# Kernel tuning notes

Measured on AMD Instinct MI355X. Metric: run time of the kernel, lower is better.

## Reference

```python
import jax, jax.numpy as jnp
import numpy as np

N, S, D = 16, 32, 256      # batch, seq_len, hidden_size
B = 4                      # sample_size (Monte-Carlo beams)
CH = 4 * D                 # cell_hidden_dim = 4*hidden (hard-coded in __init__)
EPS = 1e-20


def _ln(x, g, b):
    m = x.mean(-1, keepdims=True)
    v = ((x - m) ** 2).mean(-1, keepdims=True)
    return (x - m) / jnp.sqrt(v + 1e-5) * g + b


def _masked_softmax(logits, mask):
    p = jax.nn.softmax(logits, axis=-1)
    p = p * mask + EPS
    return p / p.sum(-1, keepdims=True)


def _cell(l, r, w1, b1, w2, b2, ln2_g, ln2_b):
    # TreeLSTM-style fused cell: Linear -> GELU -> Linear -> gates -> LayerNorm
    cat = jnp.concatenate([l, r], axis=-1)                  # (NB, s, 2D)
    inter = jax.nn.gelu(cat @ w1 + b1, approximate=False)   # (NB, s, 4D)
    contents = (inter @ w2 + b2).reshape(*l.shape[:-1], 4, D)
    gates = jax.nn.sigmoid(contents[..., 0:3, :])
    f1, f2, ig = gates[..., 0, :], gates[..., 1, :], gates[..., 2, :]
    parent = contents[..., 3, :]
    return _ln(f1 * l + f2 * r + ig * parent, ln2_g, ln2_b)


def _select(old_h, new_h, mask, accu, dec_W, dec_b, key):
    NB, Sc, Dd = new_h.shape
    old_l, old_r = old_h[:, :-1], old_h[:, 1:]
    nh = new_h * mask[:, :, None]
    pad = jnp.zeros((NB, 1, Dd), nh.dtype)
    l1 = jnp.concatenate([pad, nh[:, :-1]], axis=1)
    l2 = jnp.concatenate([pad, l1[:, :-1]], axis=1)
    r1 = jnp.concatenate([nh[:, 1:], pad], axis=1)
    r2 = jnp.concatenate([r1[:, 1:], pad], axis=1)
    win = jnp.concatenate([l2, l1, nh, r1, r2], axis=-1)    # (NB, Sc, 5D)
    logits = (win @ dec_W + dec_b)[..., 0] / np.sqrt(5 * Dd)
    # straight-through Gumbel softmax (temperature = 1)
    u = jax.random.uniform(key, logits.shape, logits.dtype)
    g = -jnp.log(-jnp.log(u + EPS) + EPS)
    y_soft = _masked_softmax(logits + g, mask)
    y_hard = jax.nn.one_hot(jnp.argmax(y_soft, axis=-1), Sc, dtype=y_soft.dtype)
    sel = jax.lax.stop_gradient(y_hard - y_soft) + y_soft
    soft_scores = jnp.sum(sel * _masked_softmax(logits, mask), axis=1)
    accu = accu + jnp.log(soft_scores + EPS)
    cs = jnp.cumsum(sel, axis=1)
    left = (1.0 - cs)[:, :, None]
    right = (cs - sel)[:, :, None]
    merged = sel[:, :, None] * new_h + left * old_l + right * old_r
    return merged, accu


def setup_inputs() -> dict:
    key = jax.random.key(0)
    ks = jax.random.split(key, 6)
    f32 = jnp.float32
    return {
        "x": jax.random.normal(ks[0], (N, S, D), f32),
        "input_mask": jnp.ones((N, S), f32),
        "word_W": jax.random.normal(ks[1], (D, D), f32) / np.sqrt(D),
        "word_b": jnp.zeros((D,), f32),
        "ln_g": jnp.ones((D,), f32),
        "ln_b": jnp.zeros((D,), f32),
        "w1": jax.random.normal(ks[2], (2 * D, CH), f32) / np.sqrt(2 * D),
        "b1": jnp.zeros((CH,), f32),
        "w2": jax.random.normal(ks[3], (CH, 4 * D), f32) / np.sqrt(CH),
        "b2": jnp.zeros((4 * D,), f32),
        "ln2_g": jnp.ones((D,), f32),
        "ln2_b": jnp.zeros((D,), f32),
        "dec_W": jax.random.normal(ks[4], (5 * D, 1), f32) / np.sqrt(5 * D),
        "dec_b": jnp.zeros((1,), f32),
    }


def reference(x, input_mask, word_W, word_b, ln_g, ln_b, w1, b1, w2, b2,
              ln2_g, ln2_b, dec_W, dec_b):
    state = _ln(x @ word_W + word_b, ln_g, ln_b)                 # (N, S, D)
    state = jnp.repeat(state[:, None], B, axis=1).reshape(N * B, S, D)
    lmask = jnp.repeat(input_mask[:, None], B, axis=1).reshape(N * B, S)
    accu = jnp.zeros((N * B,), state.dtype)
    base = jax.random.key(1234)
    # sequential tree-building recurrence; sequence axis shrinks by 1 each step
    for i in range(S - 1):
        l, r = state[:, :-1], state[:, 1:]
        new_state = _cell(l, r, w1, b1, w2, b2, ln2_g, ln2_b)
        if i < S - 2:
            new_state, new_accu = _select(state, new_state, lmask[:, i + 1:],
                                          accu, dec_W, dec_b,
                                          jax.random.fold_in(base, i))
        else:
            new_accu = accu
        done = lmask[:, i + 1]
        state = done[:, None, None] * new_state + (1.0 - done[:, None, None]) * state[:, :-1]
        accu = done * new_accu + (1.0 - done) * accu
    h = state[:, 0].reshape(N, B, D)
    scores = jax.nn.softmax(accu.reshape(N, B, 1), axis=1)
    return jnp.sum(scores * h, axis=1)                            # (N, D)
```

## Files before the change

### kernel.cpp

```cpp
#include <hip/hip_runtime.h>
#include <cstdint>
#include <cstddef>

namespace {
constexpr int kP0 = 31;
constexpr int kM0 = 496;
}

__device__ float g_state[2][64 * 32 * 256];
__device__ float g_nh[2][64 * kP0 * 256];
__device__ float g_s5[2][64 * kP0 * 5];
__device__ float g_nh0[kM0 * 256];
__device__ float g_s50[kM0 * 5];
__device__ float g_inter0[(size_t)kM0 * 1024];
__device__ float g_cont0[(size_t)kM0 * 1024];
__device__ float g_p1[4][128 * 1024];
__device__ float g_p2[4][128 * 1024];
__device__ float g_accu[64];
__device__ int g_slots[2][128];

__device__ __forceinline__ void tf2x32(uint32_t k0, uint32_t k1, uint32_t x0,
                                       uint32_t x1, uint32_t& o0, uint32_t& o1) {
  uint32_t ks2 = k0 ^ k1 ^ 0x1BD11BDAu;
  x0 += k0; x1 += k1;
#define TF_ROT(v, r) (((v) << (r)) | ((v) >> (32 - (r))))
#define TF_RD(r) { x0 += x1; x1 = TF_ROT(x1, r); x1 ^= x0; }
  TF_RD(13) TF_RD(15) TF_RD(26) TF_RD(6)   x0 += k1;  x1 += ks2 + 1u;
  TF_RD(17) TF_RD(29) TF_RD(16) TF_RD(24)  x0 += ks2; x1 += k0 + 2u;
  TF_RD(13) TF_RD(15) TF_RD(26) TF_RD(6)   x0 += k0;  x1 += k1 + 3u;
  TF_RD(17) TF_RD(29) TF_RD(16) TF_RD(24)  x0 += k1;  x1 += ks2 + 4u;
  TF_RD(13) TF_RD(15) TF_RD(26) TF_RD(6)   x0 += ks2; x1 += k0 + 5u;
  o0 = x0; o1 = x1;
#undef TF_RD
#undef TF_ROT
}

__device__ __forceinline__ float blockSum256(float v, float* red4, int tid) {
#pragma unroll
  for (int o = 32; o > 0; o >>= 1) v += __shfl_down(v, o, 64);
  __syncthreads();
  if ((tid & 63) == 0) red4[tid >> 6] = v;
  __syncthreads();
  return red4[0] + red4[1] + red4[2] + red4[3];
}
__device__ __forceinline__ float waveMax64(float v) {
#pragma unroll
  for (int o = 32; o > 0; o >>= 1) v = fmaxf(v, __shfl_xor(v, o, 64));
  return v;
}
__device__ __forceinline__ float waveSum64(float v) {
#pragma unroll
  for (int o = 32; o > 0; o >>= 1) v += __shfl_xor(v, o, 64);
  return v;
}
__device__ __forceinline__ float geluf(float v) {
  return 0.5f * v * (1.0f + erff(v * 0.70710678118654752440f));
}

__global__ __launch_bounds__(256) void k_embed(const float* __restrict__ x,
                                               const float* __restrict__ wW,
                                               const float* __restrict__ wb,
                                               const float* __restrict__ lng,
                                               const float* __restrict__ lnb) {
  int row = blockIdx.x;
  int d = threadIdx.x;
  __shared__ float xs[256];
  __shared__ float red4[4];
  xs[d] = x[row * 256 + d];
  __syncthreads();
  float acc = wb[d];
  for (int k = 0; k < 256; ++k) acc = fmaf(xs[k], wW[k * 256 + d], acc);
  float mean = blockSum256(acc, red4, d) * (1.0f / 256.0f);
  float cen = acc - mean;
  float var = blockSum256(cen * cen, red4, d) * (1.0f / 256.0f);
  float o = cen / sqrtf(var + 1e-5f) * lng[d] + lnb[d];
  int n = row >> 5, s = row & 31;
#pragma unroll
  for (int bb = 0; bb < 4; ++bb)
    g_state[0][((n * 4 + bb) * 32 + s) * 256 + d] = o;
  if (row == 0 && d < 64) g_accu[d] = 0.0f;
}


__global__ __launch_bounds__(128) void k_g1s(const float* __restrict__ w1,
                                             const float* __restrict__ b1) {
  __shared__ float As[64][20];
  __shared__ float Ws[64][132];
  const int tid = threadIdx.x;
  const int colB = blockIdx.x * 128;
  const int rowB = blockIdx.y * 16;
  const int rg = tid >> 5, cgp = tid & 31;
  const int ar = tid & 15, kq = tid >> 4;
  const int wc = tid & 31, wk = tid >> 5;
  const float* Ab;
  {
    int m = rowB + ar;
    int n = m / 31, j = m - n * 31;
    Ab = g_state[0] + (n * 4) * 8192 + j * 256;
  }
  float acc[4][4] = {};
  for (int c = 0; c < 8; ++c) {
    const int kb = c * 64;
#pragma unroll
    for (int q = 0; q < 2; ++q) {
      int kp = kq * 8 + q * 4;
      float4 a = *(const float4*)&Ab[kb + kp];
      As[kp + 0][ar] = a.x; As[kp + 1][ar] = a.y;
      As[kp + 2][ar] = a.z; As[kp + 3][ar] = a.w;
    }
#pragma unroll
    for (int q = 0; q < 16; ++q) {
      int kk = wk * 16 + q;
      *(float4*)&Ws[kk][wc * 4] =
          *(const float4*)&w1[(size_t)(kb + kk) * 1024 + colB + wc * 4];
    }
    __syncthreads();
#pragma unroll
    for (int kk = 0; kk < 64; ++kk) {
      float4 a4 = *(const float4*)&As[kk][rg * 4];
      float4 w4 = *(const float4*)&Ws[kk][cgp * 4];
      float av[4] = {a4.x, a4.y, a4.z, a4.w};
      float wv[4] = {w4.x, w4.y, w4.z, w4.w};
#pragma unroll
      for (int ri = 0; ri < 4; ++ri)
#pragma unroll
        for (int ci = 0; ci < 4; ++ci)
          acc[ri][ci] = fmaf(av[ri], wv[ci], acc[ri][ci]);
    }
    __syncthreads();
  }
  const int col = colB + cgp * 4;
  float4 bb = *(const float4*)&b1[col];
#pragma unroll
  for (int ri = 0; ri < 4; ++ri) {
    int m = rowB + rg * 4 + ri;
    float4 o;
    o.x = geluf(acc[ri][0] + bb.x); o.y = geluf(acc[ri][1] + bb.y);
    o.z = geluf(acc[ri][2] + bb.z); o.w = geluf(acc[ri][3] + bb.w);
    *(float4*)&g_inter0[(size_t)m * 1024 + col] = o;
  }
}

__global__ __launch_bounds__(128) void k_g2s(const float* __restrict__ w2) {
  __shared__ float As[64][20];
  __shared__ float Ws[64][132];
  const int tid = threadIdx.x;
  const int colB = blockIdx.x * 128;
  const int rowB = blockIdx.y * 16;
  const int rg = tid >> 5, cgp = tid & 31;
  const int ar = tid & 15, kq = tid >> 4;
  const int wc = tid & 31, wk = tid >> 5;
  const float* Ab = g_inter0 + (size_t)(rowB + ar) * 1024;
  float acc[4][4] = {};
  for (int c = 0; c < 16; ++c) {
    const int kb = c * 64;
#pragma unroll
    for (int q = 0; q < 2; ++q) {
      int kp = kq * 8 + q * 4;
      float4 a = *(const float4*)&Ab[kb + kp];
      As[kp + 0][ar] = a.x; As[kp + 1][ar] = a.y;
      As[kp + 2][ar] = a.z; As[kp + 3][ar] = a.w;
    }
#pragma unroll
    for (int q = 0; q < 16; ++q) {
      int kk = wk * 16 + q;
      *(float4*)&Ws[kk][wc * 4] =
          *(const float4*)&w2[(size_t)(kb + kk) * 1024 + colB + wc * 4];
    }
    __syncthreads();
#pragma unroll
    for (int kk = 0; kk < 64; ++kk) {
      float4 a4 = *(const float4*)&As[kk][rg * 4];
      float4 w4 = *(const float4*)&Ws[kk][cgp * 4];
      float av[4] = {a4.x, a4.y, a4.z, a4.w};
      float wv[4] = {w4.x, w4.y, w4.z, w4.w};
#pragma unroll
      for (int ri = 0; ri < 4; ++ri)
#pragma unroll
        for (int ci = 0; ci < 4; ++ci)
          acc[ri][ci] = fmaf(av[ri], wv[ci], acc[ri][ci]);
    }
    __syncthreads();
  }
  const int col = colB + cgp * 4;
#pragma unroll
  for (int ri = 0; ri < 4; ++ri) {
    int m = rowB + rg * 4 + ri;
    float4 o = {acc[ri][0], acc[ri][1], acc[ri][2], acc[ri][3]};
    *(float4*)&g_cont0[(size_t)m * 1024 + col] = o;
  }
}

__device__ __forceinline__ float4 g2t_loadA(int grow, int kpos, const float* __restrict__ b1) {
  size_t g = (size_t)grow * 1024 + kpos;
  float4 p0 = *(const float4*)&g_p1[0][g];
  float4 p1 = *(const float4*)&g_p1[1][g];
  float4 p2 = *(const float4*)&g_p1[2][g];
  float4 p3 = *(const float4*)&g_p1[3][g];
  float4 bb = *(const float4*)&b1[kpos];
  float4 r;
  r.x = geluf(p0.x + p1.x + p2.x + p3.x + bb.x);
  r.y = geluf(p0.y + p1.y + p2.y + p3.y + bb.y);
  r.z = geluf(p0.z + p1.z + p2.z + p3.z + bb.z);
  r.w = geluf(p0.w + p1.w + p2.w + p3.w + bb.w);
  return r;
}

__global__ __launch_bounds__(128) void k_g2t(const float* __restrict__ w2,
                                             const float* __restrict__ b1) {
  __shared__ float As[64][36];
  __shared__ float Ws[64][68];
  const int tid = threadIdx.x;
  const int colB = blockIdx.x * 64;
  const int rowB = blockIdx.y * 32;
  const int Ks = blockIdx.z;
  const int kb0 = Ks * 256;
  const int rg = tid >> 4, cgp = tid & 15;
  const int ar = tid & 31, kq = tid >> 5;
  const int wc = tid & 15, wk = tid >> 4;
  const int grow = rowB + ar;
  float acc[4][4] = {};
  for (int c = 0; c < 4; ++c) {
    const int kb = kb0 + c * 64;
#pragma unroll
    for (int q = 0; q < 4; ++q) {
      int kp = kq * 16 + q * 4;
      float4 a = g2t_loadA(grow, kb + kp, b1);
      As[kp + 0][ar] = a.x; As[kp + 1][ar] = a.y;
      As[kp + 2][ar] = a.z; As[kp + 3][ar] = a.w;
    }
#pragma unroll
    for (int q = 0; q < 8; ++q) {
      int kk = wk * 8 + q;
      *(float4*)&Ws[kk][wc * 4] =
          *(const float4*)&w2[(size_t)(kb + kk) * 1024 + colB + wc * 4];
    }
    __syncthreads();
#pragma unroll
    for (int kk = 0; kk < 64; ++kk) {
      float4 a4 = *(const float4*)&As[kk][rg * 4];
      float4 w4 = *(const float4*)&Ws[kk][cgp * 4];
      float av[4] = {a4.x, a4.y, a4.z, a4.w};
      float wv[4] = {w4.x, w4.y, w4.z, w4.w};
#pragma unroll
      for (int ri = 0; ri < 4; ++ri)
#pragma unroll
        for (int ci = 0; ci < 4; ++ci)
          acc[ri][ci] = fmaf(av[ri], wv[ci], acc[ri][ci]);
    }
    __syncthreads();
  }
  const int col = colB + cgp * 4;
#pragma unroll
  for (int ri = 0; ri < 4; ++ri) {
    int r = rowB + rg * 4 + ri;
    float4 o = {acc[ri][0], acc[ri][1], acc[ri][2], acc[ri][3]};
    *(float4*)&g_p2[Ks][r * 1024 + col] = o;
  }
}

__global__ __launch_bounds__(256) void k_cellfull(const float* __restrict__ imask,
                                                  const float* __restrict__ ln2g,
                                                  const float* __restrict__ ln2b,
                                                  const float* __restrict__ decW,
                                                  const float* __restrict__ b2) {
  int m = blockIdx.x;
  int d = threadIdx.x;
  int n = m / 31, j = m - n * 31;
  const float* st = g_state[0] + (n * 4) * 8192;
  const float* crow = g_cont0 + (size_t)m * 1024;
  float c0 = crow[d] + b2[d];
  float c1 = crow[256 + d] + b2[256 + d];
  float c2 = crow[512 + d] + b2[512 + d];
  float c3 = crow[768 + d] + b2[768 + d];
  float l = st[j * 256 + d];
  float r = st[(j + 1) * 256 + d];
  float f1 = 1.0f / (1.0f + expf(-c0));
  float f2 = 1.0f / (1.0f + expf(-c1));
  float ig = 1.0f / (1.0f + expf(-c2));
  float pre = f1 * l + f2 * r + ig * c3;
  __shared__ float red4[4];
  __shared__ float w5[4][5];
  float mean = blockSum256(pre, red4, d) * (1.0f / 256.0f);
  float cen = pre - mean;
  float var = blockSum256(cen * cen, red4, d) * (1.0f / 256.0f);
  float nh = cen / sqrtf(var + 1e-5f) * ln2g[d] + ln2b[d];
  g_nh0[m * 256 + d] = nh;
  float mv = imask[n * 32 + 1 + j];
  float nhm = nh * mv;
  float pv[5];
#pragma unroll
  for (int t = 0; t < 5; ++t) pv[t] = nhm * decW[t * 256 + d];
#pragma unroll
  for (int t = 0; t < 5; ++t)
#pragma unroll
    for (int o = 32; o > 0; o >>= 1) pv[t] += __shfl_down(pv[t], o, 64);
  __syncthreads();
  if ((d & 63) == 0) {
#pragma unroll
    for (int t = 0; t < 5; ++t) w5[d >> 6][t] = pv[t];
  }
  __syncthreads();
  if (d < 5) g_s50[m * 5 + d] = w5[0][d] + w5[1][d] + w5[2][d] + w5[3][d];
}

__global__ __launch_bounds__(256) void k_cm(
    const float* __restrict__ imask, const float* __restrict__ decW,
    const float* __restrict__ decb, const float* __restrict__ b2,
    const float* __restrict__ ln2g, const float* __restrict__ ln2b,
    const float* __restrict__ w1, int i, int last) {
  const int b = blockIdx.x, grp = blockIdx.y;
  const int tid = threadIdx.x, st = tid, lane = tid & 63, wv = tid >> 6;
  const int Sc = 31 - i;
  const int buf = i & 1;
  const int n32 = (b >> 2) * 32;
  __shared__ float sh_nhf[2][256];
  __shared__ float sh_s5f[2][5];
  __shared__ float sA[3][256];
  __shared__ float red4[4];
  __shared__ float w5s[4][5];
  __shared__ int sh_k;
  __shared__ float sh_sv;
  int slot0 = -1, slot1 = -1;
  if (i > 0) { slot0 = g_slots[buf][2 * b]; slot1 = g_slots[buf][2 * b + 1]; }
  const float* s5Src = (i == 0) ? (g_s50 + (b >> 2) * kP0 * 5) : (g_s5[buf] + b * kP0 * 5);
  const float* nhSrcG = (i == 0) ? (g_nh0 + (size_t)(b >> 2) * kP0 * 256)
                                 : (g_nh[buf] + (size_t)b * kP0 * 256);
  const float* stOld = g_state[buf] + b * 8192;
  float* stNew = g_state[(i + 1) & 1] + b * 8192;
  float* nhDst = g_nh[(i + 1) & 1] + (size_t)b * kP0 * 256;
  float* s5Dst = g_s5[(i + 1) & 1] + b * kP0 * 5;
  float done = imask[n32 + i + 1];

  if (i > 0) {
#pragma unroll 1
    for (int s = 0; s < 2; ++s) {
      int j = (s == 0) ? slot0 : slot1;
      if (j < 0) continue;
      int sr = 2 * b + s;
      float c[4];
#pragma unroll
      for (int q = 0; q < 4; ++q) {
        int g = sr * 1024 + q * 256 + st;
        float v = ((g_p2[0][g] + g_p2[1][g]) + g_p2[2][g]) + g_p2[3][g];
        c[q] = v + b2[q * 256 + st];
      }
      float l = stOld[j * 256 + st];
      float r = stOld[(j + 1) * 256 + st];
      float f1 = 1.0f / (1.0f + expf(-c[0]));
      float f2 = 1.0f / (1.0f + expf(-c[1]));
      float ig = 1.0f / (1.0f + expf(-c[2]));
      float pre = f1 * l + f2 * r + ig * c[3];
      float mean = blockSum256(pre, red4, st) * (1.0f / 256.0f);
      float cen = pre - mean;
      float var = blockSum256(cen * cen, red4, st) * (1.0f / 256.0f);
      float nh = cen / sqrtf(var + 1e-5f) * ln2g[st] + ln2b[st];
      sh_nhf[s][st] = nh;
      float mv = imask[n32 + i + 1 + j];
      float nhm = nh * mv;
      float pv[5];
#pragma unroll
      for (int t = 0; t < 5; ++t) pv[t] = nhm * decW[t * 256 + st];
#pragma unroll
      for (int t = 0; t < 5; ++t) {
        float v = pv[t];
#pragma unroll
        for (int o = 32; o > 0; o >>= 1) v += __shfl_down(v, o, 64);
        pv[t] = v;
      }
      __syncthreads();
      if (lane == 0) {
#pragma unroll
        for (int t = 0; t < 5; ++t) w5s[wv][t] = pv[t];
      }
      __syncthreads();
      if (st < 5) sh_s5f[s][st] = w5s[0][st] + w5s[1][st] + w5s[2][st] + w5s[3][st];
    }
  }
  __syncthreads();

  if (!last && tid < 64) {
    int j = lane;
    bool act = j < Sc;
    float mv = 0.f, lg = 0.f;
    if (act) {
      mv = imask[n32 + i + 1 + j];
      float t5 = decb[0];
      if (j >= 2) {
        int rw = j - 2;
        t5 += (i > 0 && rw == slot0) ? sh_s5f[0][0] : (i > 0 && rw == slot1) ? sh_s5f[1][0] : s5Src[rw * 5 + 0];
      }
      if (j >= 1) {
        int rw = j - 1;
        t5 += (i > 0 && rw == slot0) ? sh_s5f[0][1] : (i > 0 && rw == slot1) ? sh_s5f[1][1] : s5Src[rw * 5 + 1];
      }
      {
        int rw = j;
        t5 += (i > 0 && rw == slot0) ? sh_s5f[0][2] : (i > 0 && rw == slot1) ? sh_s5f[1][2] : s5Src[rw * 5 + 2];
      }
      if (j + 1 < Sc) {
        int rw = j + 1;
        t5 += (i > 0 && rw == slot0) ? sh_s5f[0][3] : (i > 0 && rw == slot1) ? sh_s5f[1][3] : s5Src[rw * 5 + 3];
      }
      if (j + 2 < Sc) {
        int rw = j + 2;
        t5 += (i > 0 && rw == slot0) ? sh_s5f[0][4] : (i > 0 && rw == slot1) ? sh_s5f[1][4] : s5Src[rw * 5 + 4];
      }
      lg = t5 / 35.77708763999664f;
    }
    uint32_t fk0, fk1, o0, o1;
    tf2x32(0u, 1234u, 0u, (uint32_t)i, fk0, fk1);
    uint32_t idx = (uint32_t)(b * Sc + j);
    tf2x32(fk0, fk1, 0u, idx, o0, o1);
    uint32_t bits = o0 ^ o1;
    float u = __uint_as_float((bits >> 9) | 0x3f800000u) - 1.0f;
    float gum = -logf(-logf(u + 1e-20f) + 1e-20f);
    float z = lg + gum;
    float zm = waveMax64(act ? z : -3.0e38f);
    float e = act ? expf(z - zm) : 0.f;
    float p = e / waveSum64(e);
    float y = act ? (p * mv + 1e-20f) : 0.f;
    float ys = y / waveSum64(y);
    float av = act ? ys : -1.f;
    int ai = j;
#pragma unroll
    for (int o = 32; o > 0; o >>= 1) {
      float ov = __shfl_xor(av, o, 64);
      int oi = __shfl_xor(ai, o, 64);
      if (ov > av || (ov == av && oi < ai)) { av = ov; ai = oi; }
    }
    float lm = waveMax64(act ? lg : -3.0e38f);
    float e2 = act ? expf(lg - lm) : 0.f;
    float p2 = e2 / waveSum64(e2);
    float y2 = act ? (p2 * mv + 1e-20f) : 0.f;
    float ps = y2 / waveSum64(y2);
    float ysk = __shfl(ys, ai, 64);
    float psk = __shfl(ps, ai, 64);
    float sv = (1.0f - ysk) + ysk;
    if (j == 0) {
      sh_k = ai;
      sh_sv = sv;
      if (grp == 0) {
        g_accu[b] += done * logf(sv * psk + 1e-20f);
        int s0 = -1, s1 = -1;
        if (done != 0.0f) {
          if (ai >= 1) s0 = ai - 1;
          if (ai <= Sc - 2) s1 = ai;
        }
        g_slots[(i + 1) & 1][2 * b] = s0;
        g_slots[(i + 1) & 1][2 * b + 1] = s1;
      }
    }
  }
  __syncthreads();

  if (last) {
    if (grp == 0 && wv == 0) {
      float4 ol = *(const float4*)&stOld[lane * 4];
      float4 nh4;
      if (slot0 == 0) nh4 = *(const float4*)&sh_nhf[0][lane * 4];
      else if (slot1 == 0) nh4 = *(const float4*)&sh_nhf[1][lane * 4];
      else nh4 = *(const float4*)&nhSrcG[lane * 4];
      float4 o4;
      o4.x = done * nh4.x + (1.0f - done) * ol.x;
      o4.y = done * nh4.y + (1.0f - done) * ol.y;
      o4.z = done * nh4.z + (1.0f - done) * ol.z;
      o4.w = done * nh4.w + (1.0f - done) * ol.w;
      *(float4*)&stNew[lane * 4] = o4;
    }
    return;
  }

  int k = sh_k;
  float sv = sh_sv;
#pragma unroll 1
  for (int rr = 0; rr < 2; ++rr) {
    int jrow = grp * 8 + wv * 2 + rr;
    if (jrow >= Sc) continue;
    float4 ol = *(const float4*)&stOld[jrow * 256 + lane * 4];
    float4 ov4;
    if (done != 0.0f) {
      float4 mg;
      if (jrow < k) {
        mg = ol;
      } else if (jrow == k) {
        float4 nh4 = (i > 0 && k == slot0) ? *(const float4*)&sh_nhf[0][lane * 4]
                   : (i > 0 && k == slot1) ? *(const float4*)&sh_nhf[1][lane * 4]
                   : *(const float4*)&nhSrcG[k * 256 + lane * 4];
        mg.x = sv * nh4.x + (1.0f - sv) * ol.x;
        mg.y = sv * nh4.y + (1.0f - sv) * ol.y;
        mg.z = sv * nh4.z + (1.0f - sv) * ol.z;
        mg.w = sv * nh4.w + (1.0f - sv) * ol.w;
      } else {
        float4 orr = *(const float4*)&stOld[(jrow + 1) * 256 + lane * 4];
        mg.x = (1.0f - sv) * ol.x + sv * orr.x;
        mg.y = (1.0f - sv) * ol.y + sv * orr.y;
        mg.z = (1.0f - sv) * ol.z + sv * orr.z;
        mg.w = (1.0f - sv) * ol.w + sv * orr.w;
      }
      ov4.x = done * mg.x + (1.0f - done) * ol.x;
      ov4.y = done * mg.y + (1.0f - done) * ol.y;
      ov4.z = done * mg.z + (1.0f - done) * ol.z;
      ov4.w = done * mg.w + (1.0f - done) * ol.w;
    } else {
      ov4 = ol;
    }
    *(float4*)&stNew[jrow * 256 + lane * 4] = ov4;
    if (jrow < Sc - 1) {
      int src = (done != 0.0f && jrow > k) ? jrow + 1 : jrow;
      float4 nv = (i > 0 && src == slot0) ? *(const float4*)&sh_nhf[0][lane * 4]
                : (i > 0 && src == slot1) ? *(const float4*)&sh_nhf[1][lane * 4]
                : *(const float4*)&nhSrcG[src * 256 + lane * 4];
      *(float4*)&nhDst[jrow * 256 + lane * 4] = nv;
      float mv2 = imask[n32 + i + 2 + jrow];
      float pv[5];
#pragma unroll
      for (int t = 0; t < 5; ++t) {
        const float* dw = decW + t * 256 + lane * 4;
        pv[t] = (nv.x * dw[0] + nv.y * dw[1] + nv.z * dw[2] + nv.w * dw[3]) * mv2;
      }
#pragma unroll
      for (int t = 0; t < 5; ++t) {
        float v = pv[t];
#pragma unroll
        for (int o = 32; o > 0; o >>= 1) v += __shfl_down(v, o, 64);
        pv[t] = v;
      }
      if (lane == 0) {
#pragma unroll
        for (int t = 0; t < 5; ++t) s5Dst[jrow * 5 + t] = pv[t];
      }
    }
  }

  if (done != 0.0f) {
    __syncthreads();
    {
      int d = st;
      float nhKv = (i > 0 && k == slot0) ? sh_nhf[0][d]
                 : (i > 0 && k == slot1) ? sh_nhf[1][d]
                 : nhSrcG[k * 256 + d];
#pragma unroll
      for (int t = 0; t < 3; ++t) {
        int r = k - 1 + t;
        if (r < 0 || r > Sc - 1) continue;
        float ol = stOld[r * 256 + d];
        float mg;
        if (r < k) mg = ol;
        else if (r == k) mg = sv * nhKv + (1.0f - sv) * ol;
        else mg = (1.0f - sv) * ol + sv * stOld[(r + 1) * 256 + d];
        sA[t][d] = done * mg + (1.0f - done) * ol;
      }
    }
    __syncthreads();
    const int Ks = grp;
    const int has0 = (k >= 1);
    const int has1 = (k <= Sc - 2);
    const int kb0 = Ks * 128;
    const float* A0 = (Ks < 2) ? sA[0] : sA[1];
    const float* A1 = (Ks < 2) ? sA[1] : sA[2];
    const int koff = (Ks < 2) ? kb0 : (kb0 - 256);
    const int col = st * 4;
    float a00 = 0.f, a01 = 0.f, a02 = 0.f, a03 = 0.f;
    float a10 = 0.f, a11 = 0.f, a12 = 0.f, a13 = 0.f;
    for (int kk = 0; kk < 128; ++kk) {
      float4 w = *(const float4*)&w1[(size_t)(kb0 + kk) * 1024 + col];
      float av0 = A0[koff + kk];
      float av1 = A1[koff + kk];
      a00 = fmaf(av0, w.x, a00); a01 = fmaf(av0, w.y, a01);
      a02 = fmaf(av0, w.z, a02); a03 = fmaf(av0, w.w, a03);
      a10 = fmaf(av1, w.x, a10); a11 = fmaf(av1, w.y, a11);
      a12 = fmaf(av1, w.z, a12); a13 = fmaf(av1, w.w, a13);
    }
    if (has0) {
      float4 o = {a00, a01, a02, a03};
      *(float4*)&g_p1[Ks][(2 * b + 0) * 1024 + col] = o;
    }
    if (has1) {
      float4 o = {a10, a11, a12, a13};
      *(float4*)&g_p1[Ks][(2 * b + 1) * 1024 + col] = o;
    }
  }
}

__global__ __launch_bounds__(256) void k_final(float* __restrict__ out) {
  int n = blockIdx.x, d = threadIdx.x;
  float a0 = g_accu[n * 4 + 0], a1 = g_accu[n * 4 + 1];
  float a2 = g_accu[n * 4 + 2], a3 = g_accu[n * 4 + 3];
  float mx = fmaxf(fmaxf(a0, a1), fmaxf(a2, a3));
  float e0 = expf(a0 - mx), e1 = expf(a1 - mx), e2 = expf(a2 - mx), e3 = expf(a3 - mx);
  float ssum = e0 + e1 + e2 + e3;
  const float* st1 = g_state[1];
  float h0 = st1[(n * 4 + 0) * 8192 + d];
  float h1 = st1[(n * 4 + 1) * 8192 + d];
  float h2 = st1[(n * 4 + 2) * 8192 + d];
  float h3 = st1[(n * 4 + 3) * 8192 + d];
  out[n * 256 + d] = (e0 / ssum) * h0 + (e1 / ssum) * h1 + (e2 / ssum) * h2 + (e3 / ssum) * h3;
}

extern "C" void kernel_launch(void* const* d_in, const int* in_sizes, int n_in,
                              void* d_out, int out_size, void* d_ws, size_t ws_size,
                              hipStream_t stream) {
  (void)in_sizes; (void)n_in; (void)d_ws; (void)ws_size; (void)out_size;
  const float* x = (const float*)d_in[0];
  const float* imask = (const float*)d_in[1];
  const float* wW = (const float*)d_in[2];
  const float* wb = (const float*)d_in[3];
  const float* lng = (const float*)d_in[4];
  const float* lnb = (const float*)d_in[5];
  const float* w1 = (const float*)d_in[6];
  const float* b1 = (const float*)d_in[7];
  const float* w2 = (const float*)d_in[8];
  const float* b2 = (const float*)d_in[9];
  const float* ln2g = (const float*)d_in[10];
  const float* ln2b = (const float*)d_in[11];
  const float* decW = (const float*)d_in[12];
  const float* decb = (const float*)d_in[13];
  float* out = (float*)d_out;

  k_embed<<<dim3(512), dim3(256), 0, stream>>>(x, wW, wb, lng, lnb);
  k_g1s<<<dim3(8, 31), dim3(128), 0, stream>>>(w1, b1);
  k_g2s<<<dim3(8, 31), dim3(128), 0, stream>>>(w2);
  k_cellfull<<<dim3(kM0), dim3(256), 0, stream>>>(imask, ln2g, ln2b, decW, b2);
  k_cm<<<dim3(64, 4), dim3(256), 0, stream>>>(imask, decW, decb, b2, ln2g, ln2b, w1, 0, 0);
  for (int i = 1; i <= 30; ++i) {
    k_g2t<<<dim3(16, 4, 4), dim3(128), 0, stream>>>(w2, b1);
    int lastf = (i == 30) ? 1 : 0;
    k_cm<<<dim3(64, lastf ? 1 : 4), dim3(256), 0, stream>>>(imask, decW, decb, b2,
                                                            ln2g, ln2b, w1, i, lastf);
  }
  k_final<<<dim3(16), dim3(256), 0, stream>>>(out);
}
```

Before: 1.324 ms.

## Fuse the 30-step tail recurrence into one persistent per-beam kernel

Replaces the 60 per-step launches of k_g2t and k_cm with one k_tail kernel: 64 blocks of 1024 threads, each owning a beam and looping over all 30 steps. Both cell matmuls for the two affected rows run inside the block, with partial sums, the selection scores and the slots kept in shared memory. The step-0 merge goes into a separate k_cm0 kernel. This removes launch overhead and global round-trips between steps, but each step now uses only 64 CUs, and each block re-streams the full w1 and w2 weights every step with little reuse.

Measured after the change: 2.011 ms. 1.52x slower.

```diff
diff --git a/kernel.cpp b/kernel.cpp
--- a/kernel.cpp
+++ b/kernel.cpp
@@ -14,8 +14,6 @@
 __device__ float g_s50[kM0 * 5];
 __device__ float g_inter0[(size_t)kM0 * 1024];
 __device__ float g_cont0[(size_t)kM0 * 1024];
-__device__ float g_p1[4][128 * 1024];
-__device__ float g_p2[4][128 * 1024];
 __device__ float g_accu[64];
 __device__ int g_slots[2][128];
 
@@ -42,6 +40,14 @@
   if ((tid & 63) == 0) red4[tid >> 6] = v;
   __syncthreads();
   return red4[0] + red4[1] + red4[2] + red4[3];
+}
+__device__ __forceinline__ float bs16(float v, float* red16, int tid) {
+#pragma unroll
+  for (int o = 32; o > 0; o >>= 1) v += __shfl_down(v, o, 64);
+  __syncthreads();
+  if ((tid & 63) == 0) red16[tid >> 6] = v;
+  __syncthreads();
+  return red16[0] + red16[1] + red16[2] + red16[3];
 }
 __device__ __forceinline__ float waveMax64(float v) {
 #pragma unroll
@@ -188,74 +194,6 @@
     int m = rowB + rg * 4 + ri;
     float4 o = {acc[ri][0], acc[ri][1], acc[ri][2], acc[ri][3]};
     *(float4*)&g_cont0[(size_t)m * 1024 + col] = o;
-  }
-}
-
-__device__ __forceinline__ float4 g2t_loadA(int grow, int kpos, const float* __restrict__ b1) {
-  size_t g = (size_t)grow * 1024 + kpos;
-  float4 p0 = *(const float4*)&g_p1[0][g];
-  float4 p1 = *(const float4*)&g_p1[1][g];
-  float4 p2 = *(const float4*)&g_p1[2][g];
-  float4 p3 = *(const float4*)&g_p1[3][g];
-  float4 bb = *(const float4*)&b1[kpos];
-  float4 r;
-  r.x = geluf(p0.x + p1.x + p2.x + p3.x + bb.x);
-  r.y = geluf(p0.y + p1.y + p2.y + p3.y + bb.y);
-  r.z = geluf(p0.z + p1.z + p2.z + p3.z + bb.z);
-  r.w = geluf(p0.w + p1.w + p2.w + p3.w + bb.w);
-  return r;
-}
-
-__global__ __launch_bounds__(128) void k_g2t(const float* __restrict__ w2,
-                                             const float* __restrict__ b1) {
-  __shared__ float As[64][36];
-  __shared__ float Ws[64][68];
-  const int tid = threadIdx.x;
-  const int colB = blockIdx.x * 64;
-  const int rowB = blockIdx.y * 32;
-  const int Ks = blockIdx.z;
-  const int kb0 = Ks * 256;
-  const int rg = tid >> 4, cgp = tid & 15;
-  const int ar = tid & 31, kq = tid >> 5;
-  const int wc = tid & 15, wk = tid >> 4;
-  const int grow = rowB + ar;
-  float acc[4][4] = {};
-  for (int c = 0; c < 4; ++c) {
-    const int kb = kb0 + c * 64;
-#pragma unroll
-    for (int q = 0; q < 4; ++q) {
-      int kp = kq * 16 + q * 4;
-      float4 a = g2t_loadA(grow, kb + kp, b1);
-      As[kp + 0][ar] = a.x; As[kp + 1][ar] = a.y;
-      As[kp + 2][ar] = a.z; As[kp + 3][ar] = a.w;
-    }
-#pragma unroll
-    for (int q = 0; q < 8; ++q) {
-      int kk = wk * 8 + q;
-      *(float4*)&Ws[kk][wc * 4] =
-          *(const float4*)&w2[(size_t)(kb + kk) * 1024 + colB + wc * 4];
-    }
-    __syncthreads();
-#pragma unroll
-    for (int kk = 0; kk < 64; ++kk) {
-      float4 a4 = *(const float4*)&As[kk][rg * 4];
-      float4 w4 = *(const float4*)&Ws[kk][cgp * 4];
-      float av[4] = {a4.x, a4.y, a4.z, a4.w};
-      float wv[4] = {w4.x, w4.y, w4.z, w4.w};
-#pragma unroll
-      for (int ri = 0; ri < 4; ++ri)
-#pragma unroll
-        for (int ci = 0; ci < 4; ++ci)
-          acc[ri][ci] = fmaf(av[ri], wv[ci], acc[ri][ci]);
-    }
-    __syncthreads();
-  }
-  const int col = colB + cgp * 4;
-#pragma unroll
-  for (int ri = 0; ri < 4; ++ri) {
-    int r = rowB + rg * 4 + ri;
-    float4 o = {acc[ri][0], acc[ri][1], acc[ri][2], acc[ri][3]};
-    *(float4*)&g_p2[Ks][r * 1024 + col] = o;
   }
 }
 
@@ -304,112 +242,40 @@
   if (d < 5) g_s50[m * 5 + d] = w5[0][d] + w5[1][d] + w5[2][d] + w5[3][d];
 }
 
-__global__ __launch_bounds__(256) void k_cm(
+__global__ __launch_bounds__(256) void k_cm0(
     const float* __restrict__ imask, const float* __restrict__ decW,
-    const float* __restrict__ decb, const float* __restrict__ b2,
-    const float* __restrict__ ln2g, const float* __restrict__ ln2b,
-    const float* __restrict__ w1, int i, int last) {
+    const float* __restrict__ decb, const float* __restrict__ ln2g,
+    const float* __restrict__ ln2b) {
   const int b = blockIdx.x, grp = blockIdx.y;
-  const int tid = threadIdx.x, st = tid, lane = tid & 63, wv = tid >> 6;
-  const int Sc = 31 - i;
-  const int buf = i & 1;
+  const int tid = threadIdx.x, lane = tid & 63, wv = tid >> 6;
+  const int Sc = 31;
   const int n32 = (b >> 2) * 32;
-  __shared__ float sh_nhf[2][256];
-  __shared__ float sh_s5f[2][5];
-  __shared__ float sA[3][256];
-  __shared__ float red4[4];
-  __shared__ float w5s[4][5];
   __shared__ int sh_k;
   __shared__ float sh_sv;
-  int slot0 = -1, slot1 = -1;
-  if (i > 0) { slot0 = g_slots[buf][2 * b]; slot1 = g_slots[buf][2 * b + 1]; }
-  const float* s5Src = (i == 0) ? (g_s50 + (b >> 2) * kP0 * 5) : (g_s5[buf] + b * kP0 * 5);
-  const float* nhSrcG = (i == 0) ? (g_nh0 + (size_t)(b >> 2) * kP0 * 256)
-                                 : (g_nh[buf] + (size_t)b * kP0 * 256);
-  const float* stOld = g_state[buf] + b * 8192;
-  float* stNew = g_state[(i + 1) & 1] + b * 8192;
-  float* nhDst = g_nh[(i + 1) & 1] + (size_t)b * kP0 * 256;
-  float* s5Dst = g_s5[(i + 1) & 1] + b * kP0 * 5;
-  float done = imask[n32 + i + 1];
-
-  if (i > 0) {
-#pragma unroll 1
-    for (int s = 0; s < 2; ++s) {
-      int j = (s == 0) ? slot0 : slot1;
-      if (j < 0) continue;
-      int sr = 2 * b + s;
-      float c[4];
-#pragma unroll
-      for (int q = 0; q < 4; ++q) {
-        int g = sr * 1024 + q * 256 + st;
-        float v = ((g_p2[0][g] + g_p2[1][g]) + g_p2[2][g]) + g_p2[3][g];
-        c[q] = v + b2[q * 256 + st];
-      }
-      float l = stOld[j * 256 + st];
-      float r = stOld[(j + 1) * 256 + st];
-      float f1 = 1.0f / (1.0f + expf(-c[0]));
-      float f2 = 1.0f / (1.0f + expf(-c[1]));
-      float ig = 1.0f / (1.0f + expf(-c[2]));
-      float pre = f1 * l + f2 * r + ig * c[3];
-      float mean = blockSum256(pre, red4, st) * (1.0f / 256.0f);
-      float cen = pre - mean;
-      float var = blockSum256(cen * cen, red4, st) * (1.0f / 256.0f);
-      float nh = cen / sqrtf(var + 1e-5f) * ln2g[st] + ln2b[st];
-      sh_nhf[s][st] = nh;
-      float mv = imask[n32 + i + 1 + j];
-      float nhm = nh * mv;
-      float pv[5];
-#pragma unroll
-      for (int t = 0; t < 5; ++t) pv[t] = nhm * decW[t * 256 + st];
-#pragma unroll
-      for (int t = 0; t < 5; ++t) {
-        float v = pv[t];
-#pragma unroll
-        for (int o = 32; o > 0; o >>= 1) v += __shfl_down(v, o, 64);
-        pv[t] = v;
-      }
-      __syncthreads();
-      if (lane == 0) {
-#pragma unroll
-        for (int t = 0; t < 5; ++t) w5s[wv][t] = pv[t];
-      }
-      __syncthreads();
-      if (st < 5) sh_s5f[s][st] = w5s[0][st] + w5s[1][st] + w5s[2][st] + w5s[3][st];
-    }
-  }
-  __syncthreads();
-
-  if (!last && tid < 64) {
+  const float* s5Src = g_s50 + (b >> 2) * kP0 * 5;
+  const float* nhSrcG = g_nh0 + (size_t)(b >> 2) * kP0 * 256;
+  const float* stOld = g_state[0] + b * 8192;
+  float* stNew = g_state[1] + b * 8192;
+  float* nhDst = g_nh[1] + (size_t)b * kP0 * 256;
+  float* s5Dst = g_s5[1] + b * kP0 * 5;
+  float done = imask[n32 + 1];
+
+  if (tid < 64) {
     int j = lane;
     bool act = j < Sc;
     float mv = 0.f, lg = 0.f;
     if (act) {
-      mv = imask[n32 + i + 1 + j];
+      mv = imask[n32 + 1 + j];
       float t5 = decb[0];
-      if (j >= 2) {
-        int rw = j - 2;
-        t5 += (i > 0 && rw == slot0) ? sh_s5f[0][0] : (i > 0 && rw == slot1) ? sh_s5f[1][0] : s5Src[rw * 5 + 0];
-      }
-      if (j >= 1) {
-        int rw = j - 1;
-        t5 += (i > 0 && rw == slot0) ? sh_s5f[0][1] : (i > 0 && rw == slot1) ? sh_s5f[1][1] : s5Src[rw * 5 + 1];
-      }
-      {
-        int rw = j;
-        t5 += (i > 0 && rw == slot0) ? sh_s5f[0][2] : (i > 0 && rw == slot1) ? sh_s5f[1][2] : s5Src[rw * 5 + 2];
-      }
-      if (j + 1 < Sc) {
-        int rw = j + 1;
-        t5 += (i > 0 && rw == slot0) ? sh_s5f[0][3] : (i > 0 && rw == slot1) ? sh_s5f[1][3] : s5Src[rw * 5 + 3];
-      }
-      if (j + 2 < Sc) {
-        int rw = j + 2;
-        t5 += (i > 0 && rw == slot0) ? sh_s5f[0][4] : (i > 0 && rw == slot1) ? sh_s5f[1][4] : s5Src[rw * 5 + 4];
-      }
+      if (j >= 2) t5 += s5Src[(j - 2) * 5 + 0];
+      if (j >= 1) t5 += s5Src[(j - 1) * 5 + 1];
+      t5 += s5Src[j * 5 + 2];
+      if (j + 1 < Sc) t5 += s5Src[(j + 1) * 5 + 3];
+      if (j + 2 < Sc) t5 += s5Src[(j + 2) * 5 + 4];
       lg = t5 / 35.77708763999664f;
     }
     uint32_t fk0, fk1, o0, o1;
-    tf2x32(0u, 1234u, 0u, (uint32_t)i, fk0, fk1);
+    tf2x32(0u, 1234u, 0u, 0u, fk0, fk1);
     uint32_t idx = (uint32_t)(b * Sc + j);
     tf2x32(fk0, fk1, 0u, idx, o0, o1);
     uint32_t bits = o0 ^ o1;
@@ -447,140 +313,384 @@
           if (ai >= 1) s0 = ai - 1;
           if (ai <= Sc - 2) s1 = ai;
         }
-        g_slots[(i + 1) & 1][2 * b] = s0;
-        g_slots[(i + 1) & 1][2 * b + 1] = s1;
-      }
-    }
-  }
-  __syncthreads();
-
-  if (last) {
-    if (grp == 0 && wv == 0) {
-      float4 ol = *(const float4*)&stOld[lane * 4];
-      float4 nh4;
-      if (slot0 == 0) nh4 = *(const float4*)&sh_nhf[0][lane * 4];
-      else if (slot1 == 0) nh4 = *(const float4*)&sh_nhf[1][lane * 4];
-      else nh4 = *(const float4*)&nhSrcG[lane * 4];
-      float4 o4;
-      o4.x = done * nh4.x + (1.0f - done) * ol.x;
-      o4.y = done * nh4.y + (1.0f - done) * ol.y;
-      o4.z = done * nh4.z + (1.0f - done) * ol.z;
-      o4.w = done * nh4.w + (1.0f - done) * ol.w;
-      *(float4*)&stNew[lane * 4] = o4;
-    }
-    return;
-  }
+        g_slots[1][2 * b] = s0;
+        g_slots[1][2 * b + 1] = s1;
+      }
+    }
+  }
+  __syncthreads();
 
   int k = sh_k;
   float sv = sh_sv;
+  {
+    int jrow = grp * 4 + wv;
+    if (jrow < Sc) {
+      float4 ol = *(const float4*)&stOld[jrow * 256 + lane * 4];
+      float4 ov4;
+      if (done != 0.0f) {
+        float4 mg;
+        if (jrow < k) {
+          mg = ol;
+        } else if (jrow == k) {
+          float4 nh4 = *(const float4*)&nhSrcG[k * 256 + lane * 4];
+          mg.x = sv * nh4.x + (1.0f - sv) * ol.x;
+          mg.y = sv * nh4.y + (1.0f - sv) * ol.y;
+          mg.z = sv * nh4.z + (1.0f - sv) * ol.z;
+          mg.w = sv * nh4.w + (1.0f - sv) * ol.w;
+        } else {
+          float4 orr = *(const float4*)&stOld[(jrow + 1) * 256 + lane * 4];
+          mg.x = (1.0f - sv) * ol.x + sv * orr.x;
+          mg.y = (1.0f - sv) * ol.y + sv * orr.y;
+          mg.z = (1.0f - sv) * ol.z + sv * orr.z;
+          mg.w = (1.0f - sv) * ol.w + sv * orr.w;
+        }
+        ov4.x = done * mg.x + (1.0f - done) * ol.x;
+        ov4.y = done * mg.y + (1.0f - done) * ol.y;
+        ov4.z = done * mg.z + (1.0f - done) * ol.z;
+        ov4.w = done * mg.w + (1.0f - done) * ol.w;
+      } else {
+        ov4 = ol;
+      }
+      *(float4*)&stNew[jrow * 256 + lane * 4] = ov4;
+      if (jrow < Sc - 1) {
+        int src = (done != 0.0f && jrow > k) ? jrow + 1 : jrow;
+        float4 nv = *(const float4*)&nhSrcG[src * 256 + lane * 4];
+        *(float4*)&nhDst[jrow * 256 + lane * 4] = nv;
+        float mv2 = imask[n32 + 2 + jrow];
+        float pv[5];
+#pragma unroll
+        for (int t = 0; t < 5; ++t) {
+          const float* dw = decW + t * 256 + lane * 4;
+          pv[t] = (nv.x * dw[0] + nv.y * dw[1] + nv.z * dw[2] + nv.w * dw[3]) * mv2;
+        }
+#pragma unroll
+        for (int t = 0; t < 5; ++t) {
+          float v = pv[t];
+#pragma unroll
+          for (int o = 32; o > 0; o >>= 1) v += __shfl_down(v, o, 64);
+          pv[t] = v;
+        }
+        if (lane == 0) {
+#pragma unroll
+          for (int t = 0; t < 5; ++t) s5Dst[jrow * 5 + t] = pv[t];
+        }
+      }
+    }
+  }
+}
+
+__global__ __launch_bounds__(1024, 1) void k_tail(
+    const float* __restrict__ imask, const float* __restrict__ decW,
+    const float* __restrict__ decb, const float* __restrict__ b1,
+    const float* __restrict__ b2, const float* __restrict__ ln2g,
+    const float* __restrict__ ln2b, const float* __restrict__ w1,
+    const float* __restrict__ w2) {
+  const int b = blockIdx.x;
+  const int tid = threadIdx.x;
+  const int lane = tid & 63, wv = tid >> 6;
+  const int n32 = (b >> 2) * 32;
+  __shared__ float S[4][2][1024];
+  __shared__ float IC[2][1024];
+  __shared__ float As2[2][512];
+  __shared__ float sh_nhf[2][256];
+  __shared__ float sh_s5f[2][5];
+  __shared__ float s5buf[2][32][5];
+  __shared__ float red16[16];
+  __shared__ float w5s[4][5];
+  __shared__ int sh_slot0, sh_slot1;
+  __shared__ int sh_k;
+  __shared__ float sh_sv;
+  __shared__ float sh_accu;
+
+  if (tid < 150) s5buf[1][tid / 5][tid % 5] = g_s5[1][b * kP0 * 5 + tid];
+  if (tid == 0) {
+    sh_slot0 = g_slots[1][2 * b];
+    sh_slot1 = g_slots[1][2 * b + 1];
+    sh_accu = g_accu[b];
+  }
+  __syncthreads();
+
 #pragma unroll 1
-  for (int rr = 0; rr < 2; ++rr) {
-    int jrow = grp * 8 + wv * 2 + rr;
-    if (jrow >= Sc) continue;
-    float4 ol = *(const float4*)&stOld[jrow * 256 + lane * 4];
-    float4 ov4;
-    if (done != 0.0f) {
-      float4 mg;
-      if (jrow < k) {
-        mg = ol;
-      } else if (jrow == k) {
-        float4 nh4 = (i > 0 && k == slot0) ? *(const float4*)&sh_nhf[0][lane * 4]
-                   : (i > 0 && k == slot1) ? *(const float4*)&sh_nhf[1][lane * 4]
-                   : *(const float4*)&nhSrcG[k * 256 + lane * 4];
-        mg.x = sv * nh4.x + (1.0f - sv) * ol.x;
-        mg.y = sv * nh4.y + (1.0f - sv) * ol.y;
-        mg.z = sv * nh4.z + (1.0f - sv) * ol.z;
-        mg.w = sv * nh4.w + (1.0f - sv) * ol.w;
-      } else {
-        float4 orr = *(const float4*)&stOld[(jrow + 1) * 256 + lane * 4];
-        mg.x = (1.0f - sv) * ol.x + sv * orr.x;
-        mg.y = (1.0f - sv) * ol.y + sv * orr.y;
-        mg.z = (1.0f - sv) * ol.z + sv * orr.z;
-        mg.w = (1.0f - sv) * ol.w + sv * orr.w;
-      }
-      ov4.x = done * mg.x + (1.0f - done) * ol.x;
-      ov4.y = done * mg.y + (1.0f - done) * ol.y;
-      ov4.z = done * mg.z + (1.0f - done) * ol.z;
-      ov4.w = done * mg.w + (1.0f - done) * ol.w;
+  for (int i = 1; i <= 30; ++i) {
+    const int Sc = 31 - i;
+    const int buf = i & 1;
+    const int last = (i == 30);
+    const float* stOld = g_state[buf] + b * 8192;
+    float* stNew = g_state[buf ^ 1] + b * 8192;
+    const float* nhSrc = g_nh[buf] + (size_t)b * kP0 * 256;
+    float* nhDst = g_nh[buf ^ 1] + (size_t)b * kP0 * 256;
+    const float done = imask[n32 + i + 1];
+    const int slot0 = sh_slot0, slot1 = sh_slot1;
+
+    if (slot0 >= 0 || slot1 >= 0) {
+      {
+        int j0 = slot0 >= 0 ? slot0 : 0;
+        int j1 = slot1 >= 0 ? slot1 : 0;
+        if (tid < 512) As2[0][tid] = stOld[j0 * 256 + tid];
+        else As2[1][tid - 512] = stOld[j1 * 256 + (tid - 512)];
+      }
+      __syncthreads();
+      {
+        const int Ks = tid >> 8, c4 = tid & 255;
+        float a00=0.f,a01=0.f,a02=0.f,a03=0.f,a10=0.f,a11=0.f,a12=0.f,a13=0.f;
+        const float* wp = w1 + (size_t)(Ks * 128) * 1024 + c4 * 4;
+        const float* A0 = &As2[0][Ks * 128];
+        const float* A1 = &As2[1][Ks * 128];
+#pragma unroll 4
+        for (int kk = 0; kk < 128; ++kk) {
+          float4 w = *(const float4*)(wp + (size_t)kk * 1024);
+          float av0 = A0[kk], av1 = A1[kk];
+          a00 = fmaf(av0, w.x, a00); a01 = fmaf(av0, w.y, a01);
+          a02 = fmaf(av0, w.z, a02); a03 = fmaf(av0, w.w, a03);
+          a10 = fmaf(av1, w.x, a10); a11 = fmaf(av1, w.y, a11);
+          a12 = fmaf(av1, w.z, a12); a13 = fmaf(av1, w.w, a13);
+        }
+        float4 o0 = {a00, a01, a02, a03};
+        float4 o1 = {a10, a11, a12, a13};
+        *(float4*)&S[Ks][0][c4 * 4] = o0;
+        *(float4*)&S[Ks][1][c4 * 4] = o1;
+      }
+      __syncthreads();
+#pragma unroll
+      for (int e = tid; e < 2048; e += 1024) {
+        int s = e >> 10, col = e & 1023;
+        IC[s][col] = geluf((((S[0][s][col] + S[1][s][col]) + S[2][s][col]) + S[3][s][col]) + b1[col]);
+      }
+      __syncthreads();
+      {
+        const int Ks = tid >> 8, c4 = tid & 255;
+        float a00=0.f,a01=0.f,a02=0.f,a03=0.f,a10=0.f,a11=0.f,a12=0.f,a13=0.f;
+        const float* wp = w2 + (size_t)(Ks * 256) * 1024 + c4 * 4;
+        const float* I0 = &IC[0][Ks * 256];
+        const float* I1 = &IC[1][Ks * 256];
+#pragma unroll 4
+        for (int kk = 0; kk < 256; ++kk) {
+          float4 w = *(const float4*)(wp + (size_t)kk * 1024);
+          float iv0 = I0[kk], iv1 = I1[kk];
+          a00 = fmaf(iv0, w.x, a00); a01 = fmaf(iv0, w.y, a01);
+          a02 = fmaf(iv0, w.z, a02); a03 = fmaf(iv0, w.w, a03);
+          a10 = fmaf(iv1, w.x, a10); a11 = fmaf(iv1, w.y, a11);
+          a12 = fmaf(iv1, w.z, a12); a13 = fmaf(iv1, w.w, a13);
+        }
+        float4 o0 = {a00, a01, a02, a03};
+        float4 o1 = {a10, a11, a12, a13};
+        __syncthreads();
+        *(float4*)&S[0][0][0 * 4] = *(float4*)&S[0][0][0 * 4];
+        *(float4*)&IC[0][0] = *(float4*)&IC[0][0];
+        {
+          float4 t0 = o0, t1 = o1;
+          *(float4*)&S[Ks][0][c4 * 4] = t0;
+          *(float4*)&S[Ks][1][c4 * 4] = t1;
+        }
+      }
+      __syncthreads();
+#pragma unroll
+      for (int e = tid; e < 2048; e += 1024) {
+        int s = e >> 10, col = e & 1023;
+        IC[s][col] = (((S[0][s][col] + S[1][s][col]) + S[2][s][col]) + S[3][s][col]);
+      }
+      __syncthreads();
+#pragma unroll 1
+      for (int s = 0; s < 2; ++s) {
+        int j = (s == 0) ? slot0 : slot1;
+        if (j < 0) continue;
+        const int d = tid & 255;
+        const bool act = tid < 256;
+        float pre = 0.f;
+        if (act) {
+          float c0 = IC[s][d] + b2[d];
+          float c1 = IC[s][256 + d] + b2[256 + d];
+          float c2 = IC[s][512 + d] + b2[512 + d];
+          float c3 = IC[s][768 + d] + b2[768 + d];
+          float l = stOld[j * 256 + d];
+          float r = stOld[(j + 1) * 256 + d];
+          float f1 = 1.0f / (1.0f + expf(-c0));
+          float f2 = 1.0f / (1.0f + expf(-c1));
+          float ig = 1.0f / (1.0f + expf(-c2));
+          pre = f1 * l + f2 * r + ig * c3;
+        }
+        float mean = bs16(pre, red16, tid) * (1.0f / 256.0f);
+        float cen = pre - mean;
+        float var = bs16(cen * cen, red16, tid) * (1.0f / 256.0f);
+        float nh = cen / sqrtf(var + 1e-5f) * ln2g[d] + ln2b[d];
+        if (act) sh_nhf[s][d] = nh;
+        float mv = imask[n32 + i + 1 + j];
+        float nhm = nh * mv;
+        float pv[5];
+#pragma unroll
+        for (int t = 0; t < 5; ++t) pv[t] = nhm * decW[t * 256 + d];
+#pragma unroll
+        for (int t = 0; t < 5; ++t) {
+          float v = pv[t];
+#pragma unroll
+          for (int o = 32; o > 0; o >>= 1) v += __shfl_down(v, o, 64);
+          pv[t] = v;
+        }
+        __syncthreads();
+        if (lane == 0 && wv < 4) {
+#pragma unroll
+          for (int t = 0; t < 5; ++t) w5s[wv][t] = pv[t];
+        }
+        __syncthreads();
+        if (tid < 5) sh_s5f[s][tid] = w5s[0][tid] + w5s[1][tid] + w5s[2][tid] + w5s[3][tid];
+        __syncthreads();
+      }
+    }
+    __syncthreads();
+
+    if (!last && tid < 64) {
+      int j = lane;
+      bool act = j < Sc;
+      float mv = 0.f, lg = 0.f;
+      if (act) {
+        mv = imask[n32 + i + 1 + j];
+        float t5 = decb[0];
+        if (j >= 2) {
+          int rw = j - 2;
+          t5 += (rw == slot0) ? sh_s5f[0][0] : (rw == slot1) ? sh_s5f[1][0] : s5buf[buf][rw][0];
+        }
+        if (j >= 1) {
+          int rw = j - 1;
+          t5 += (rw == slot0) ? sh_s5f[0][1] : (rw == slot1) ? sh_s5f[1][1] : s5buf[buf][rw][1];
+        }
+        {
+          int rw = j;
+          t5 += (rw == slot0) ? sh_s5f[0][2] : (rw == slot1) ? sh_s5f[1][2] : s5buf[buf][rw][2];
+        }
+        if (j + 1 < Sc) {
+          int rw = j + 1;
+          t5 += (rw == slot0) ? sh_s5f[0][3] : (rw == slot1) ? sh_s5f[1][3] : s5buf[buf][rw][3];
+        }
+        if (j + 2 < Sc) {
+          int rw = j + 2;
+          t5 += (rw == slot0) ? sh_s5f[0][4] : (rw == slot1) ? sh_s5f[1][4] : s5buf[buf][rw][4];
+        }
+        lg = t5 / 35.77708763999664f;
+      }
+      uint32_t fk0, fk1, o0, o1;
+      tf2x32(0u, 1234u, 0u, (uint32_t)i, fk0, fk1);
+      uint32_t idx = (uint32_t)(b * Sc + j);
+      tf2x32(fk0, fk1, 0u, idx, o0, o1);
+      uint32_t bits = o0 ^ o1;
+      float u = __uint_as_float((bits >> 9) | 0x3f800000u) - 1.0f;
+      float gum = -logf(-logf(u + 1e-20f) + 1e-20f);
+      float z = lg + gum;
+      float zm = waveMax64(act ? z : -3.0e38f);
+      float e = act ? expf(z - zm) : 0.f;
+      float p = e / waveSum64(e);
+      float y = act ? (p * mv + 1e-20f) : 0.f;
+      float ys = y / waveSum64(y);
+      float av = act ? ys : -1.f;
+      int ai = j;
+#pragma unroll
+      for (int o = 32; o > 0; o >>= 1) {
+        float ov = __shfl_xor(av, o, 64);
+        int oi = __shfl_xor(ai, o, 64);
+        if (ov > av || (ov == av && oi < ai)) { av = ov; ai = oi; }
+      }
+      float lm = waveMax64(act ? lg : -3.0e38f);
+      float e2 = act ? expf(lg - lm) : 0.f;
+      float p2 = e2 / waveSum64(e2);
+      float y2 = act ? (p2 * mv + 1e-20f) : 0.f;
+      float ps = y2 / waveSum64(y2);
+      float ysk = __shfl(ys, ai, 64);
+      float psk = __shfl(ps, ai, 64);
+      float sv = (1.0f - ysk) + ysk;
+      if (j == 0) {
+        sh_k = ai;
+        sh_sv = sv;
+        sh_accu += done * logf(sv * psk + 1e-20f);
+        int s0 = -1, s1 = -1;
+        if (done != 0.0f) {
+          if (ai >= 1) s0 = ai - 1;
+          if (ai <= Sc - 2) s1 = ai;
+        }
+        sh_slot0 = s0;
+        sh_slot1 = s1;
+      }
+    }
+    __syncthreads();
+
+    if (last) {
+      if (wv == 0) {
+        float4 ol = *(const float4*)&stOld[lane * 4];
+        float4 nh4;
+        if (slot0 == 0) nh4 = *(const float4*)&sh_nhf[0][lane * 4];
+        else if (slot1 == 0) nh4 = *(const float4*)&sh_nhf[1][lane * 4];
+        else nh4 = *(const float4*)&nhSrc[lane * 4];
+        float4 o4;
+        o4.x = done * nh4.x + (1.0f - done) * ol.x;
+        o4.y = done * nh4.y + (1.0f - done) * ol.y;
+        o4.z = done * nh4.z + (1.0f - done) * ol.z;
+        o4.w = done * nh4.w + (1.0f - done) * ol.w;
+        *(float4*)&stNew[lane * 4] = o4;
+      }
     } else {
-      ov4 = ol;
-    }
-    *(float4*)&stNew[jrow * 256 + lane * 4] = ov4;
-    if (jrow < Sc - 1) {
-      int src = (done != 0.0f && jrow > k) ? jrow + 1 : jrow;
-      float4 nv = (i > 0 && src == slot0) ? *(const float4*)&sh_nhf[0][lane * 4]
-                : (i > 0 && src == slot1) ? *(const float4*)&sh_nhf[1][lane * 4]
-                : *(const float4*)&nhSrcG[src * 256 + lane * 4];
-      *(float4*)&nhDst[jrow * 256 + lane * 4] = nv;
-      float mv2 = imask[n32 + i + 2 + jrow];
-      float pv[5];
-#pragma unroll
-      for (int t = 0; t < 5; ++t) {
-        const float* dw = decW + t * 256 + lane * 4;
-        pv[t] = (nv.x * dw[0] + nv.y * dw[1] + nv.z * dw[2] + nv.w * dw[3]) * mv2;
-      }
-#pragma unroll
-      for (int t = 0; t < 5; ++t) {
-        float v = pv[t];
-#pragma unroll
-        for (int o = 32; o > 0; o >>= 1) v += __shfl_down(v, o, 64);
-        pv[t] = v;
-      }
-      if (lane == 0) {
-#pragma unroll
-        for (int t = 0; t < 5; ++t) s5Dst[jrow * 5 + t] = pv[t];
-      }
-    }
-  }
-
-  if (done != 0.0f) {
-    __syncthreads();
-    {
-      int d = st;
-      float nhKv = (i > 0 && k == slot0) ? sh_nhf[0][d]
-                 : (i > 0 && k == slot1) ? sh_nhf[1][d]
-                 : nhSrcG[k * 256 + d];
-#pragma unroll
-      for (int t = 0; t < 3; ++t) {
-        int r = k - 1 + t;
-        if (r < 0 || r > Sc - 1) continue;
-        float ol = stOld[r * 256 + d];
-        float mg;
-        if (r < k) mg = ol;
-        else if (r == k) mg = sv * nhKv + (1.0f - sv) * ol;
-        else mg = (1.0f - sv) * ol + sv * stOld[(r + 1) * 256 + d];
-        sA[t][d] = done * mg + (1.0f - done) * ol;
-      }
-    }
-    __syncthreads();
-    const int Ks = grp;
-    const int has0 = (k >= 1);
-    const int has1 = (k <= Sc - 2);
-    const int kb0 = Ks * 128;
-    const float* A0 = (Ks < 2) ? sA[0] : sA[1];
-    const float* A1 = (Ks < 2) ? sA[1] : sA[2];
-    const int koff = (Ks < 2) ? kb0 : (kb0 - 256);
-    const int col = st * 4;
-    float a00 = 0.f, a01 = 0.f, a02 = 0.f, a03 = 0.f;
-    float a10 = 0.f, a11 = 0.f, a12 = 0.f, a13 = 0.f;
-    for (int kk = 0; kk < 128; ++kk) {
-      float4 w = *(const float4*)&w1[(size_t)(kb0 + kk) * 1024 + col];
-      float av0 = A0[koff + kk];
-      float av1 = A1[koff + kk];
-      a00 = fmaf(av0, w.x, a00); a01 = fmaf(av0, w.y, a01);
-      a02 = fmaf(av0, w.z, a02); a03 = fmaf(av0, w.w, a03);
-      a10 = fmaf(av1, w.x, a10); a11 = fmaf(av1, w.y, a11);
-      a12 = fmaf(av1, w.z, a12); a13 = fmaf(av1, w.w, a13);
-    }
-    if (has0) {
-      float4 o = {a00, a01, a02, a03};
-      *(float4*)&g_p1[Ks][(2 * b + 0) * 1024 + col] = o;
-    }
-    if (has1) {
-      float4 o = {a10, a11, a12, a13};
-      *(float4*)&g_p1[Ks][(2 * b + 1) * 1024 + col] = o;
-    }
-  }
+      int k = sh_k;
+      float sv = sh_sv;
+#pragma unroll 1
+      for (int rr = 0; rr < 2; ++rr) {
+        int jrow = wv + 16 * rr;
+        if (jrow >= Sc) continue;
+        float4 ol = *(const float4*)&stOld[jrow * 256 + lane * 4];
+        float4 ov4;
+        if (done != 0.0f) {
+          float4 mg;
+          if (jrow < k) {
+            mg = ol;
+          } else if (jrow == k) {
+            float4 nh4 = (k == slot0) ? *(const float4*)&sh_nhf[0][lane * 4]
+                       : (k == slot1) ? *(const float4*)&sh_nhf[1][lane * 4]
+                       : *(const float4*)&nhSrc[k * 256 + lane * 4];
+            mg.x = sv * nh4.x + (1.0f - sv) * ol.x;
+            mg.y = sv * nh4.y + (1.0f - sv) * ol.y;
+            mg.z = sv * nh4.z + (1.0f - sv) * ol.z;
+            mg.w = sv * nh4.w + (1.0f - sv) * ol.w;
+          } else {
+            float4 orr = *(const float4*)&stOld[(jrow + 1) * 256 + lane * 4];
+            mg.x = (1.0f - sv) * ol.x + sv * orr.x;
+            mg.y = (1.0f - sv) * ol.y + sv * orr.y;
+            mg.z = (1.0f - sv) * ol.z + sv * orr.z;
+            mg.w = (1.0f - sv) * ol.w + sv * orr.w;
+          }
+          ov4.x = done * mg.x + (1.0f - done) * ol.x;
+          ov4.y = done * mg.y + (1.0f - done) * ol.y;
+          ov4.z = done * mg.z + (1.0f - done) * ol.z;
+          ov4.w = done * mg.w + (1.0f - done) * ol.w;
+        } else {
+          ov4 = ol;
+        }
+        *(float4*)&stNew[jrow * 256 + lane * 4] = ov4;
+        if (jrow < Sc - 1) {
+          int src = (done != 0.0f && jrow > k) ? jrow + 1 : jrow;
+          float4 nv = (src == slot0) ? *(const float4*)&sh_nhf[0][lane * 4]
+                    : (src == slot1) ? *(const float4*)&sh_nhf[1][lane * 4]
+                    : *(const float4*)&nhSrc[src * 256 + lane * 4];
+          *(float4*)&nhDst[jrow * 256 + lane * 4] = nv;
+          float mv2 = imask[n32 + i + 2 + jrow];
+          float pv[5];
+#pragma unroll
+          for (int t = 0; t < 5; ++t) {
+            const float* dw = decW + t * 256 + lane * 4;
+            pv[t] = (nv.x * dw[0] + nv.y * dw[1] + nv.z * dw[2] + nv.w * dw[3]) * mv2;
+          }
+#pragma unroll
+          for (int t = 0; t < 5; ++t) {
+            float v = pv[t];
+#pragma unroll
+            for (int o = 32; o > 0; o >>= 1) v += __shfl_down(v, o, 64);
+            pv[t] = v;
+          }
+          if (lane == 0) {
+#pragma unroll
+            for (int t = 0; t < 5; ++t) s5buf[buf ^ 1][jrow][t] = pv[t];
+          }
+        }
+      }
+      __syncthreads();
+    }
+  }
+  if (tid == 0) g_accu[b] = sh_accu;
 }
 
 __global__ __launch_bounds__(256) void k_final(float* __restrict__ out) {
@@ -622,12 +732,8 @@
   k_g1s<<<dim3(8, 31), dim3(128), 0, stream>>>(w1, b1);
   k_g2s<<<dim3(8, 31), dim3(128), 0, stream>>>(w2);
   k_cellfull<<<dim3(kM0), dim3(256), 0, stream>>>(imask, ln2g, ln2b, decW, b2);
-  k_cm<<<dim3(64, 4), dim3(256), 0, stream>>>(imask, decW, decb, b2, ln2g, ln2b, w1, 0, 0);
-  for (int i = 1; i <= 30; ++i) {
-    k_g2t<<<dim3(16, 4, 4), dim3(128), 0, stream>>>(w2, b1);
-    int lastf = (i == 30) ? 1 : 0;
-    k_cm<<<dim3(64, lastf ? 1 : 4), dim3(256), 0, stream>>>(imask, decW, decb, b2,
-                                                            ln2g, ln2b, w1, i, lastf);
-  }
+  k_cm0<<<dim3(64, 8), dim3(256), 0, stream>>>(imask, decW, decb, ln2g, ln2b);
+  k_tail<<<dim3(64), dim3(1024), 0, stream>>>(imask, decW, decb, b1, b2, ln2g,
+                                              ln2b, w1, w2);
   k_final<<<dim3(16), dim3(256), 0, stream>>>(out);
 }
```
